# Performance work log

Hardware: AMD Instinct MI355X
Metric: run time of the kernel (lower is better)

## Reference

```python
import jax, jax.numpy as jnp
import numpy as np

B, N, D = 32, 32768, 128

def setup_inputs() -> dict:
    key = jax.random.key(0)
    k1, k2, k3 = jax.random.split(key, 3)
    inputs = jax.random.normal(k1, (B, D), dtype=jnp.float32)
    # alphas must be in (0,1): variance = 1 - alpha
    alphas = jax.random.uniform(k2, (B,), dtype=jnp.float32, minval=0.05, maxval=0.95)
    data_batch = jax.random.normal(k3, (N, D), dtype=jnp.float32)
    return {"inputs": inputs, "alphas": alphas, "data_batch": data_batch}

def reference(inputs, alphas, data_batch):
    # inputs: [B, D], alphas: [B], data_batch: [N, D]
    d = inputs.shape[-1]
    sqrt_a = jnp.sqrt(alphas)[:, None]          # [B, 1]
    var = (1.0 - alphas)[:, None]                # [B, 1]
    # means = sqrt(alpha) * data -> [B, N, D]; squared distance summed over D
    diff = inputs[:, None, :] - sqrt_a[:, :, None] * data_batch[None]  # [B, N, D]
    sq = jnp.sum(diff * diff, axis=-1)           # [B, N]
    # logits summed over feature dim: -(0.5*D*log(var) + 0.5/var * sq)
    logits = -(0.5 * d * jnp.log(var) + 0.5 / var * sq)  # [B, N]
    probs = jax.nn.softmax(logits, axis=1)       # [B, N]
    x0 = probs @ data_batch                      # [B, D]
    return (inputs - sqrt_a * x0) / jnp.sqrt(var)
```

## Files before the change

### kernel.cpp

```cpp
#include <hip/hip_runtime.h>
#include <math.h>

#define BB 32
#define DD 128
#define NN 32768

#define NB 512
#define RPB 64
#define NP NB
#define WS_MS_OFF ((size_t)BB * NB * DD)

typedef __attribute__((ext_vector_type(8))) short bf16x8;
typedef __attribute__((ext_vector_type(4))) float f32x4;

#define O_RH   0
#define O_RL   16384
#define O_INH  32768
#define O_INL  40960
#define O_RT   49152
#define O_D1   65536
#define O_NRM  75776
#define O_PT   O_INH
#define O_X0   O_RH
#define ARENA  76032

__device__ __forceinline__ unsigned bf16_rne(float x) {
    unsigned u = __builtin_bit_cast(unsigned, x);
    return (u + 0x7FFFu + ((u >> 16) & 1u)) >> 16;
}
__device__ __forceinline__ float bf16f(unsigned h) {
    return __builtin_bit_cast(float, h << 16);
}
__device__ __forceinline__ unsigned pk2(float a, float b) {
    return bf16_rne(a) | (bf16_rne(b) << 16);
}

__global__ __launch_bounds__(256) void bayes_k1(
    const float* __restrict__ inputs, const float* __restrict__ alphas,
    const float* __restrict__ data, float* __restrict__ ws)
{
    __shared__ __align__(16) char arena[ARENA];

    const int tid  = threadIdx.x;
    const int lane = tid & 63;
    const int wv   = tid >> 6;
    const int ln   = lane & 15;
    const int g    = lane >> 4;
    const int bid  = blockIdx.x;

    {
        const int r = tid >> 2, c4 = tid & 3;
        const float4* gp = (const float4*)(data + ((size_t)bid * RPB + r) * DD + c4 * 32);
        float v[32];
        #pragma unroll
        for (int i = 0; i < 8; ++i) {
            const float4 t4 = gp[i];
            v[4*i+0] = t4.x; v[4*i+1] = t4.y; v[4*i+2] = t4.z; v[4*i+3] = t4.w;
        }
        float nn = 0.0f;
        #pragma unroll
        for (int i = 0; i < 32; ++i) nn = fmaf(v[i], v[i], nn);
        nn += __shfl_xor(nn, 1);
        nn += __shfl_xor(nn, 2);
        if (c4 == 0) *(float*)(arena + O_NRM + r * 4) = nn;

        const int swz = (r & 7) << 4;
        #pragma unroll
        for (int u = 0; u < 4; ++u) {
            unsigned hw[4], lw[4];
            #pragma unroll
            for (int j = 0; j < 4; ++j) {
                const float a = v[u*8 + 2*j], b = v[u*8 + 2*j + 1];
                const unsigned ah = bf16_rne(a), bh = bf16_rne(b);
                hw[j] = ah | (bh << 16);
                lw[j] = pk2(a - bf16f(ah), b - bf16f(bh));
            }
            const int go = (c4 * 64 + u * 16) ^ swz;
            *(uint4*)(arena + O_RH + r * 256 + go) = make_uint4(hw[0], hw[1], hw[2], hw[3]);
            *(uint4*)(arena + O_RL + r * 256 + go) = make_uint4(lw[0], lw[1], lw[2], lw[3]);
        }
    }

    {
        const int b = tid >> 3, c8 = tid & 7;
        const float4* gp = (const float4*)(inputs + b * DD + c8 * 16);
        float v[16];
        #pragma unroll
        for (int i = 0; i < 4; ++i) {
            const float4 t4 = gp[i];
            v[4*i+0] = t4.x; v[4*i+1] = t4.y; v[4*i+2] = t4.z; v[4*i+3] = t4.w;
        }
        const int swz = (b & 7) << 4;
        #pragma unroll
        for (int u = 0; u < 2; ++u) {
            unsigned hw[4], lw[4];
            #pragma unroll
            for (int j = 0; j < 4; ++j) {
                const float a = v[u*8 + 2*j], bb = v[u*8 + 2*j + 1];
                const unsigned ah = bf16_rne(a), bh = bf16_rne(bb);
                hw[j] = ah | (bh << 16);
                lw[j] = pk2(a - bf16f(ah), bb - bf16f(bh));
            }
            const int go = (c8 * 32 + u * 16) ^ swz;
            *(uint4*)(arena + O_INH + b * 256 + go) = make_uint4(hw[0], hw[1], hw[2], hw[3]);
            *(uint4*)(arena + O_INL + b * 256 + go) = make_uint4(lw[0], lw[1], lw[2], lw[3]);
        }
    }

    {
        const int d = tid >> 1, rh = tid & 1;
        const float* gc = data + ((size_t)bid * RPB + rh * 32) * DD + d;
        const int swz = (d & 7) << 4;
        #pragma unroll
        for (int u = 0; u < 4; ++u) {
            unsigned w[4];
            #pragma unroll
            for (int j = 0; j < 4; ++j)
                w[j] = pk2(gc[(u*8 + 2*j) * DD], gc[(u*8 + 2*j + 1) * DD]);
            *(uint4*)(arena + O_RT + d * 128 + ((rh * 64 + u * 16) ^ swz)) =
                make_uint4(w[0], w[1], w[2], w[3]);
        }
    }
    __syncthreads();

    const int ni = wv & 1;
    const int kh = wv >> 1;
    f32x4 acc1[4];
    #pragma unroll
    for (int mt = 0; mt < 4; ++mt)
        #pragma unroll
        for (int i = 0; i < 4; ++i) acc1[mt][i] = 0.0f;

    #pragma unroll
    for (int ks = 0; ks < 2; ++ks) {
        const int kbyte = kh * 128 + ks * 64 + g * 16;
        const int n = ni * 16 + ln;
        const bf16x8 Bh = *(const bf16x8*)(arena + O_INH + n * 256 + (kbyte ^ ((n & 7) << 4)));
        const bf16x8 Bl = *(const bf16x8*)(arena + O_INL + n * 256 + (kbyte ^ ((n & 7) << 4)));
        #pragma unroll
        for (int mt = 0; mt < 4; ++mt) {
            const int r = mt * 16 + ln;
            const bf16x8 Ah = *(const bf16x8*)(arena + O_RH + r * 256 + (kbyte ^ ((r & 7) << 4)));
            const bf16x8 Al = *(const bf16x8*)(arena + O_RL + r * 256 + (kbyte ^ ((r & 7) << 4)));
            acc1[mt] = __builtin_amdgcn_mfma_f32_16x16x32_bf16(Ah, Bh, acc1[mt], 0, 0, 0);
            acc1[mt] = __builtin_amdgcn_mfma_f32_16x16x32_bf16(Al, Bh, acc1[mt], 0, 0, 0);
            acc1[mt] = __builtin_amdgcn_mfma_f32_16x16x32_bf16(Ah, Bl, acc1[mt], 0, 0, 0);
        }
    }
    if (kh == 1) {
        #pragma unroll
        for (int mt = 0; mt < 4; ++mt)
            *(f32x4*)(arena + O_D1 + ((ni * 4 + mt) * 16 + ln) * 80 + g * 16) = acc1[mt];
    }
    __syncthreads();

    if (kh == 0) {
        const int b = ni * 16 + ln;
        #pragma unroll
        for (int mt = 0; mt < 4; ++mt) {
            const f32x4 o = *(const f32x4*)(arena + O_D1 + ((ni * 4 + mt) * 16 + ln) * 80 + g * 16);
            #pragma unroll
            for (int i = 0; i < 4; ++i) acc1[mt][i] += o[i];
        }
        const float alpha = alphas[b];
        const float var = 1.0f - alpha;
        const float c1 = sqrtf(alpha) / var;
        const float c2 = 0.5f * alpha / var;

        float lg[4][4];
        float mx = -1e30f;
        #pragma unroll
        for (int mt = 0; mt < 4; ++mt) {
            const f32x4 nr4 = *(const f32x4*)(arena + O_NRM + (mt * 16 + g * 4) * 4);
            #pragma unroll
            for (int i = 0; i < 4; ++i) {
                lg[mt][i] = fmaf(c1, acc1[mt][i], -c2 * nr4[i]);
                mx = fmaxf(mx, lg[mt][i]);
            }
        }
        mx = fmaxf(mx, __shfl_xor(mx, 16));
        mx = fmaxf(mx, __shfl_xor(mx, 32));

        float ss = 0.0f;
        const int swz = (b & 7) << 4;
        #pragma unroll
        for (int mt = 0; mt < 4; ++mt) {
            float e0 = __expf(lg[mt][0] - mx), e1 = __expf(lg[mt][1] - mx);
            float e2 = __expf(lg[mt][2] - mx), e3 = __expf(lg[mt][3] - mx);
            ss += (e0 + e1) + (e2 + e3);
            *(uint2*)(arena + O_PT + b * 128 + ((mt * 32 + g * 8) ^ swz)) =
                make_uint2(pk2(e0, e1), pk2(e2, e3));
        }
        ss += __shfl_xor(ss, 16);
        ss += __shfl_xor(ss, 32);
        if (g == 0)
            *(float2*)(ws + WS_MS_OFF + ((size_t)b * NB + bid) * 2) = make_float2(mx, ss);
    }
    __syncthreads();

    {
        f32x4 acc2[2][2];
        #pragma unroll
        for (int a = 0; a < 2; ++a)
            #pragma unroll
            for (int c = 0; c < 2; ++c)
                #pragma unroll
                for (int i = 0; i < 4; ++i) acc2[a][c][i] = 0.0f;

        #pragma unroll
        for (int ks = 0; ks < 2; ++ks) {
            bf16x8 Bp[2];
            #pragma unroll
            for (int nt = 0; nt < 2; ++nt) {
                const int b2 = nt * 16 + ln;
                Bp[nt] = *(const bf16x8*)(arena + O_PT + b2 * 128 +
                                          ((ks * 64 + g * 16) ^ ((b2 & 7) << 4)));
            }
            #pragma unroll
            for (int mt2 = 0; mt2 < 2; ++mt2) {
                const int d = wv * 32 + mt2 * 16 + ln;
                const bf16x8 Ar = *(const bf16x8*)(arena + O_RT + d * 128 +
                                                   ((ks * 64 + g * 16) ^ ((d & 7) << 4)));
                #pragma unroll
                for (int nt = 0; nt < 2; ++nt)
                    acc2[mt2][nt] = __builtin_amdgcn_mfma_f32_16x16x32_bf16(Ar, Bp[nt], acc2[mt2][nt], 0, 0, 0);
            }
        }
        #pragma unroll
        for (int mt2 = 0; mt2 < 2; ++mt2)
            #pragma unroll
            for (int nt = 0; nt < 2; ++nt) {
                const int b = nt * 16 + ln;
                const int d0 = wv * 32 + mt2 * 16 + g * 4;
                *(f32x4*)(arena + O_X0 + b * 512 + ((d0 * 4) ^ ((b & 7) << 4))) = acc2[mt2][nt];
            }
    }
    __syncthreads();

    {
        const int b = tid >> 3, c8 = tid & 7;
        const int swz = (b & 7) << 4;
        float* dst = ws + ((size_t)b * NB + bid) * DD + c8 * 16;
        #pragma unroll
        for (int u = 0; u < 4; ++u) {
            const f32x4 v = *(const f32x4*)(arena + O_X0 + b * 512 + ((c8 * 64 + u * 16) ^ swz));
            *(f32x4*)(dst + u * 4) = v;
        }
    }
}

__global__ __launch_bounds__(256) void bayes_k2(
    const float* __restrict__ inputs, const float* __restrict__ alphas,
    const float* __restrict__ ws, float* __restrict__ out)
{
    const int b   = blockIdx.x >> 2;
    const int dq  = blockIdx.x & 3;
    const int tid = threadIdx.x;

    __shared__ float e_s[NP];
    __shared__ float red_s[16];
    __shared__ float part[8][32];

    float mi[2], si[2];
    #pragma unroll
    for (int q = 0; q < 2; ++q) {
        const float2 v = *(const float2*)(ws + WS_MS_OFF + ((size_t)b * NP + tid + q * 256) * 2);
        mi[q] = v.x; si[q] = v.y;
    }

    float mm = fmaxf(mi[0], mi[1]);
    #pragma unroll
    for (int off = 1; off <= 32; off <<= 1) mm = fmaxf(mm, __shfl_xor(mm, off));
    if ((tid & 63) == 0) red_s[tid >> 6] = mm;
    __syncthreads();
    const float M = fmaxf(fmaxf(red_s[0], red_s[1]), fmaxf(red_s[2], red_s[3]));

    float ss = 0.0f;
    #pragma unroll
    for (int q = 0; q < 2; ++q) {
        const float ei = __expf(mi[q] - M);
        e_s[tid + q * 256] = ei;
        ss = fmaf(si[q], ei, ss);
    }
    #pragma unroll
    for (int off = 1; off <= 32; off <<= 1) ss += __shfl_xor(ss, off);
    if ((tid & 63) == 0) red_s[8 + (tid >> 6)] = ss;
    __syncthreads();
    const float S = (red_s[8] + red_s[9]) + (red_s[10] + red_s[11]);

    const int dd = tid & 31, ii = tid >> 5;
    const int d  = dq * 32 + dd;
    const float* xb = ws + (size_t)b * NP * DD + d;
    float xa = 0.0f, xbv = 0.0f, xc = 0.0f, xd = 0.0f;
    #pragma unroll 2
    for (int k = 0; k < 64; k += 4) {
        const int i0 = ii + (k + 0) * 8;
        const int i1 = ii + (k + 1) * 8;
        const int i2 = ii + (k + 2) * 8;
        const int i3 = ii + (k + 3) * 8;
        xa  = fmaf(e_s[i0], xb[(size_t)i0 * DD], xa);
        xbv = fmaf(e_s[i1], xb[(size_t)i1 * DD], xbv);
        xc  = fmaf(e_s[i2], xb[(size_t)i2 * DD], xc);
        xd  = fmaf(e_s[i3], xb[(size_t)i3 * DD], xd);
    }
    part[ii][dd] = (xa + xbv) + (xc + xd);
    __syncthreads();

    if (tid < 32) {
        float x0 = 0.0f;
        #pragma unroll
        for (int p = 0; p < 8; ++p) x0 += part[p][tid];
        x0 /= S;
        const float alpha = alphas[b];
        const float sa  = sqrtf(alpha);
        const float var = 1.0f - alpha;
        const int dout  = dq * 32 + tid;
        out[b * DD + dout] = (inputs[b * DD + dout] - sa * x0) / sqrtf(var);
    }
}

extern "C" void kernel_launch(void* const* d_in, const int* in_sizes, int n_in,
                              void* d_out, int out_size, void* d_ws, size_t ws_size,
                              hipStream_t stream)
{
    const float* inputs = (const float*)d_in[0];
    const float* alphas = (const float*)d_in[1];
    const float* data   = (const float*)d_in[2];
    float* out = (float*)d_out;
    float* ws  = (float*)d_ws;

    bayes_k1<<<NB, 256, 0, stream>>>(inputs, alphas, data, ws);
    bayes_k2<<<BB * 4, 256, 0, stream>>>(inputs, alphas, ws, out);
}
```

Before: 80.72 us.

## Split first GEMM by data rows per wave and widen second-kernel grid

The distance GEMM stage now gives each wave its own 16 data rows over the full K dimension, instead of splitting K across wave pairs and reducing through shared memory. Results go to a padded shared tile that two waves transpose-read for the softmax, which also lets the probabilities be stored as wider 16-byte packs. The reduction kernel launches eight blocks per batch row instead of four, each covering 16 features, to raise parallelism in the memory-bound combine. The cost is a padded scalar LDS transpose and half of the waves sitting idle during the softmax.

```diff
diff --git a/kernel.cpp b/kernel.cpp
--- a/kernel.cpp
+++ b/kernel.cpp
@@ -19,10 +19,10 @@
 #define O_INL  40960
 #define O_RT   49152
 #define O_D1   65536
-#define O_NRM  75776
+#define O_NRM  73984
 #define O_PT   O_INH
 #define O_X0   O_RH
-#define ARENA  76032
+#define ARENA  74240
 
 __device__ __forceinline__ unsigned bf16_rne(float x) {
     unsigned u = __builtin_bit_cast(unsigned, x);
@@ -123,76 +123,71 @@
     }
     __syncthreads();
 
-    const int ni = wv & 1;
-    const int kh = wv >> 1;
-    f32x4 acc1[4];
-    #pragma unroll
-    for (int mt = 0; mt < 4; ++mt)
-        #pragma unroll
-        for (int i = 0; i < 4; ++i) acc1[mt][i] = 0.0f;
-
-    #pragma unroll
-    for (int ks = 0; ks < 2; ++ks) {
-        const int kbyte = kh * 128 + ks * 64 + g * 16;
-        const int n = ni * 16 + ln;
-        const bf16x8 Bh = *(const bf16x8*)(arena + O_INH + n * 256 + (kbyte ^ ((n & 7) << 4)));
-        const bf16x8 Bl = *(const bf16x8*)(arena + O_INL + n * 256 + (kbyte ^ ((n & 7) << 4)));
-        #pragma unroll
-        for (int mt = 0; mt < 4; ++mt) {
-            const int r = mt * 16 + ln;
+    {
+        const int r = wv * 16 + ln;
+        f32x4 acc1[2];
+        #pragma unroll
+        for (int nt = 0; nt < 2; ++nt)
+            #pragma unroll
+            for (int i = 0; i < 4; ++i) acc1[nt][i] = 0.0f;
+
+        #pragma unroll
+        for (int ks = 0; ks < 4; ++ks) {
+            const int kbyte = ks * 64 + g * 16;
             const bf16x8 Ah = *(const bf16x8*)(arena + O_RH + r * 256 + (kbyte ^ ((r & 7) << 4)));
             const bf16x8 Al = *(const bf16x8*)(arena + O_RL + r * 256 + (kbyte ^ ((r & 7) << 4)));
-            acc1[mt] = __builtin_amdgcn_mfma_f32_16x16x32_bf16(Ah, Bh, acc1[mt], 0, 0, 0);
-            acc1[mt] = __builtin_amdgcn_mfma_f32_16x16x32_bf16(Al, Bh, acc1[mt], 0, 0, 0);
-            acc1[mt] = __builtin_amdgcn_mfma_f32_16x16x32_bf16(Ah, Bl, acc1[mt], 0, 0, 0);
-        }
-    }
-    if (kh == 1) {
-        #pragma unroll
-        for (int mt = 0; mt < 4; ++mt)
-            *(f32x4*)(arena + O_D1 + ((ni * 4 + mt) * 16 + ln) * 80 + g * 16) = acc1[mt];
-    }
-    __syncthreads();
-
-    if (kh == 0) {
-        const int b = ni * 16 + ln;
-        #pragma unroll
-        for (int mt = 0; mt < 4; ++mt) {
-            const f32x4 o = *(const f32x4*)(arena + O_D1 + ((ni * 4 + mt) * 16 + ln) * 80 + g * 16);
-            #pragma unroll
-            for (int i = 0; i < 4; ++i) acc1[mt][i] += o[i];
-        }
+            #pragma unroll
+            for (int nt = 0; nt < 2; ++nt) {
+                const int n = nt * 16 + ln;
+                const bf16x8 Bh = *(const bf16x8*)(arena + O_INH + n * 256 + (kbyte ^ ((n & 7) << 4)));
+                const bf16x8 Bl = *(const bf16x8*)(arena + O_INL + n * 256 + (kbyte ^ ((n & 7) << 4)));
+                acc1[nt] = __builtin_amdgcn_mfma_f32_16x16x32_bf16(Ah, Bh, acc1[nt], 0, 0, 0);
+                acc1[nt] = __builtin_amdgcn_mfma_f32_16x16x32_bf16(Al, Bh, acc1[nt], 0, 0, 0);
+                acc1[nt] = __builtin_amdgcn_mfma_f32_16x16x32_bf16(Ah, Bl, acc1[nt], 0, 0, 0);
+            }
+        }
+        #pragma unroll
+        for (int nt = 0; nt < 2; ++nt)
+            #pragma unroll
+            for (int i = 0; i < 4; ++i)
+                *(float*)(arena + O_D1 + ((wv * 16 + g * 4 + i) * 33 + nt * 16 + ln) * 4) = acc1[nt][i];
+    }
+    __syncthreads();
+
+    if (wv < 2) {
+        const int b = wv * 16 + ln;
         const float alpha = alphas[b];
         const float var = 1.0f - alpha;
         const float c1 = sqrtf(alpha) / var;
         const float c2 = 0.5f * alpha / var;
 
-        float lg[4][4];
+        float lg[16];
         float mx = -1e30f;
         #pragma unroll
-        for (int mt = 0; mt < 4; ++mt) {
-            const f32x4 nr4 = *(const f32x4*)(arena + O_NRM + (mt * 16 + g * 4) * 4);
-            #pragma unroll
-            for (int i = 0; i < 4; ++i) {
-                lg[mt][i] = fmaf(c1, acc1[mt][i], -c2 * nr4[i]);
-                mx = fmaxf(mx, lg[mt][i]);
-            }
+        for (int j = 0; j < 16; ++j) {
+            const int r = g * 16 + j;
+            const float L  = *(const float*)(arena + O_D1 + (r * 33 + b) * 4);
+            const float nr = *(const float*)(arena + O_NRM + r * 4);
+            lg[j] = fmaf(c1, L, -c2 * nr);
+            mx = fmaxf(mx, lg[j]);
         }
         mx = fmaxf(mx, __shfl_xor(mx, 16));
         mx = fmaxf(mx, __shfl_xor(mx, 32));
 
+        float e[16];
         float ss = 0.0f;
-        const int swz = (b & 7) << 4;
-        #pragma unroll
-        for (int mt = 0; mt < 4; ++mt) {
-            float e0 = __expf(lg[mt][0] - mx), e1 = __expf(lg[mt][1] - mx);
-            float e2 = __expf(lg[mt][2] - mx), e3 = __expf(lg[mt][3] - mx);
-            ss += (e0 + e1) + (e2 + e3);
-            *(uint2*)(arena + O_PT + b * 128 + ((mt * 32 + g * 8) ^ swz)) =
-                make_uint2(pk2(e0, e1), pk2(e2, e3));
-        }
+        #pragma unroll
+        for (int j = 0; j < 16; ++j) { e[j] = __expf(lg[j] - mx); ss += e[j]; }
         ss += __shfl_xor(ss, 16);
         ss += __shfl_xor(ss, 32);
+
+        const int swz = (b & 7) << 4;
+        #pragma unroll
+        for (int jj = 0; jj < 2; ++jj) {
+            *(uint4*)(arena + O_PT + b * 128 + ((g * 32 + jj * 16) ^ swz)) =
+                make_uint4(pk2(e[jj*8+0], e[jj*8+1]), pk2(e[jj*8+2], e[jj*8+3]),
+                           pk2(e[jj*8+4], e[jj*8+5]), pk2(e[jj*8+6], e[jj*8+7]));
+        }
         if (g == 0)
             *(float2*)(ws + WS_MS_OFF + ((size_t)b * NB + bid) * 2) = make_float2(mx, ss);
     }
@@ -253,13 +248,13 @@
     const float* __restrict__ inputs, const float* __restrict__ alphas,
     const float* __restrict__ ws, float* __restrict__ out)
 {
-    const int b   = blockIdx.x >> 2;
-    const int dq  = blockIdx.x & 3;
+    const int b   = blockIdx.x >> 3;
+    const int seg = blockIdx.x & 7;
     const int tid = threadIdx.x;
 
     __shared__ float e_s[NP];
     __shared__ float red_s[16];
-    __shared__ float part[8][32];
+    __shared__ float part[16][17];
 
     float mi[2], si[2];
     #pragma unroll
@@ -288,16 +283,16 @@
     __syncthreads();
     const float S = (red_s[8] + red_s[9]) + (red_s[10] + red_s[11]);
 
-    const int dd = tid & 31, ii = tid >> 5;
-    const int d  = dq * 32 + dd;
+    const int dd = tid & 15, ii = tid >> 4;
+    const int d  = seg * 16 + dd;
     const float* xb = ws + (size_t)b * NP * DD + d;
     float xa = 0.0f, xbv = 0.0f, xc = 0.0f, xd = 0.0f;
     #pragma unroll 2
-    for (int k = 0; k < 64; k += 4) {
-        const int i0 = ii + (k + 0) * 8;
-        const int i1 = ii + (k + 1) * 8;
-        const int i2 = ii + (k + 2) * 8;
-        const int i3 = ii + (k + 3) * 8;
+    for (int k = 0; k < 32; k += 4) {
+        const int i0 = ii + (k + 0) * 16;
+        const int i1 = ii + (k + 1) * 16;
+        const int i2 = ii + (k + 2) * 16;
+        const int i3 = ii + (k + 3) * 16;
         xa  = fmaf(e_s[i0], xb[(size_t)i0 * DD], xa);
         xbv = fmaf(e_s[i1], xb[(size_t)i1 * DD], xbv);
         xc  = fmaf(e_s[i2], xb[(size_t)i2 * DD], xc);
@@ -306,15 +301,15 @@
     part[ii][dd] = (xa + xbv) + (xc + xd);
     __syncthreads();
 
-    if (tid < 32) {
+    if (tid < 16) {
         float x0 = 0.0f;
         #pragma unroll
-        for (int p = 0; p < 8; ++p) x0 += part[p][tid];
+        for (int p = 0; p < 16; ++p) x0 += part[p][tid];
         x0 /= S;
         const float alpha = alphas[b];
         const float sa  = sqrtf(alpha);
         const float var = 1.0f - alpha;
-        const int dout  = dq * 32 + tid;
+        const int dout  = seg * 16 + tid;
         out[b * DD + dout] = (inputs[b * DD + dout] - sa * x0) / sqrtf(var);
     }
 }
@@ -330,5 +325,5 @@
     float* ws  = (float*)d_ws;
 
     bayes_k1<<<NB, 256, 0, stream>>>(inputs, alphas, data, ws);
-    bayes_k2<<<BB * 4, 256, 0, stream>>>(inputs, alphas, ws, out);
-}
+    bayes_k2<<<BB * 8, 256, 0, stream>>>(inputs, alphas, ws, out);
+}
```

Result: no change. 80.80 us (+0.1%).
